# Kernel tuning notes

Hardware: AMD Instinct MI355X
Metric: run time of the kernel (lower is better)

Reference implementation:

```python
import jax, jax.numpy as jnp
import numpy as np

EMB_DIM = 2048
NUM_HEADS = 16
HEAD_DIM = EMB_DIM // NUM_HEADS  # 128
B, T = 4, 2048


def setup_inputs() -> dict:
    key = jax.random.key(0)
    ks = jax.random.split(key, 6)
    s = lambda fan_in: 1.0 / np.sqrt(fan_in)
    return {
        "x": jax.random.normal(ks[0], (B, T, EMB_DIM), dtype=jnp.float32),
        # weights stored [in, out] so forward is x @ W
        "Wq": jax.random.normal(ks[1], (EMB_DIM, EMB_DIM), dtype=jnp.float32) * s(EMB_DIM),
        "Wk": jax.random.normal(ks[2], (EMB_DIM, HEAD_DIM), dtype=jnp.float32) * s(EMB_DIM),
        "Wv": jax.random.normal(ks[3], (EMB_DIM, HEAD_DIM), dtype=jnp.float32) * s(EMB_DIM),
        "Wo": jax.random.normal(ks[4], (EMB_DIM, EMB_DIM), dtype=jnp.float32) * s(EMB_DIM),
        "bo": jax.random.normal(ks[5], (EMB_DIM,), dtype=jnp.float32) * 0.01,
    }


def reference(x, Wq, Wk, Wv, Wo, bo):
    Bsz, Tlen, C = x.shape
    H, D = NUM_HEADS, HEAD_DIM
    q = (x @ Wq).reshape(Bsz, Tlen, H, D)          # [B,T,H,D]
    k = x @ Wk                                      # [B,T,D] (single shared head)
    v = x @ Wv                                      # [B,T,D]
    # MQA: K/V broadcast over heads via einsum (no expand materialization)
    scores = jnp.einsum("bihd,bjd->bhij", q, k) / jnp.sqrt(jnp.float32(D))
    i = jnp.arange(Tlen)[:, None]
    j = jnp.arange(Tlen)[None, :]
    causal = j <= i                                  # attend to past & self
    scores = jnp.where(causal, scores, -jnp.inf)
    attn = jax.nn.softmax(scores, axis=-1)           # [B,H,T,T]
    out = jnp.einsum("bhij,bjd->bihd", attn, v).reshape(Bsz, Tlen, C)
    return out @ Wo + bo
```

## Files before the change

### kernel.cpp

```cpp
#include <hip/hip_runtime.h>
#include <stdint.h>

typedef __attribute__((ext_vector_type(8))) short short8;
typedef __attribute__((ext_vector_type(4))) float floatx4;

#define TLEN 2048
#define BATCH 4
#define EMB 2048
#define NHEADS 16
#define HDIM 128
#define MROWS (BATCH * TLEN)
#define QTILES (TLEN / 64)

__device__ __forceinline__ ushort f2bf(float f) {
    union { float f; uint32_t u; } v; v.f = f;
    uint32_t u = v.u;
    return (ushort)((u + 0x7fffu + ((u >> 16) & 1u)) >> 16);
}

__device__ __forceinline__ uint32_t cvt_pk_bf16(float a, float b) {
    uint32_t r;
    asm volatile("v_cvt_pk_bf16_f32 %0, %1, %2" : "=v"(r) : "v"(a), "v"(b));
    return r;
}

__device__ __forceinline__ void async_copy16(const ushort* g, ushort* l) {
    __builtin_amdgcn_global_load_lds(
        (const __attribute__((address_space(1))) uint32_t*)g,
        (__attribute__((address_space(3))) uint32_t*)l, 16, 0, 0);
}

__global__ __launch_bounds__(256) void cast_bf16_kernel(const float* __restrict__ in,
                                                        ushort* __restrict__ out, int n) {
    int i = (blockIdx.x * 256 + threadIdx.x) * 4;
    if (i >= n) return;
    float4 f = *(const float4*)(in + i);
    ushort4 o;
    o.x = f2bf(f.x); o.y = f2bf(f.y); o.z = f2bf(f.z); o.w = f2bf(f.w);
    *(ushort4*)(out + i) = o;
}

__global__ void transpose_cast_kernel(const float* __restrict__ in, ushort* __restrict__ out,
                                      int R, int Cc) {
    __shared__ float tile[32][33];
    int x = blockIdx.x * 32 + threadIdx.x;
    int y0 = blockIdx.y * 32;
#pragma unroll
    for (int i = 0; i < 4; i++) {
        int y = y0 + threadIdx.y + i * 8;
        tile[threadIdx.y + i * 8][threadIdx.x] = in[(size_t)y * Cc + x];
    }
    __syncthreads();
    int xo = y0 + threadIdx.x;
#pragma unroll
    for (int i = 0; i < 4; i++) {
        int yo = blockIdx.x * 32 + threadIdx.y + i * 8;
        out[(size_t)yo * R + xo] = f2bf(tile[threadIdx.x][threadIdx.y + i * 8]);
    }
}

template <int MODE>
__global__ __launch_bounds__(256) void gemm_bt_kernel(const ushort* __restrict__ A,
                                                      const ushort* __restrict__ Bt,
                                                      void* __restrict__ Cp,
                                                      void* __restrict__ Cp2,
                                                      const float* __restrict__ bias,
                                                      int M, int N, int K) {
    __shared__ ushort As[128 * 64];
    __shared__ ushort Bs[128 * 64];
    int tid = threadIdx.x;
    int wid = tid >> 6, lane = tid & 63;
    int quad = lane >> 4, l15 = lane & 15;

    int nwg = gridDim.x * gridDim.y;
    int wg = blockIdx.y * gridDim.x + blockIdx.x;
    int cpx = nwg >> 3;
    int swz = (wg & 7) * cpx + (wg >> 3);
    int bx = swz % gridDim.x, by = swz / gridDim.x;

    int m0 = by * 128;
    int n0 = bx * 128;
    int rm = (wid >> 1) * 64;
    int cn = (wid & 1) * 64;
    int grow = lane >> 3;
    int gcol = (lane & 7) * 8;

    floatx4 acc[4][4];
#pragma unroll
    for (int i = 0; i < 4; i++)
#pragma unroll
        for (int j = 0; j < 4; j++)
#pragma unroll
            for (int r = 0; r < 4; r++) acc[i][j][r] = 0.f;

    for (int kk = 0; kk < K; kk += 64) {
#pragma unroll
        for (int c = 0; c < 4; c++) {
            int chunk = wid * 4 + c;
            int row = chunk * 8 + grow;
            async_copy16(A + (size_t)(m0 + row) * K + kk + gcol, &As[chunk * 512]);
            async_copy16(Bt + (size_t)(n0 + row) * K + kk + gcol, &Bs[chunk * 512]);
        }
        __syncthreads();
#pragma unroll
        for (int ks = 0; ks < 64; ks += 32) {
            short8 af[4], bf[4];
#pragma unroll
            for (int i = 0; i < 4; i++)
                af[i] = *(const short8*)(&As[(rm + i * 16 + l15) * 64 + ks + quad * 8]);
#pragma unroll
            for (int j = 0; j < 4; j++)
                bf[j] = *(const short8*)(&Bs[(cn + j * 16 + l15) * 64 + ks + quad * 8]);
#pragma unroll
            for (int i = 0; i < 4; i++)
#pragma unroll
                for (int j = 0; j < 4; j++)
                    acc[i][j] = __builtin_amdgcn_mfma_f32_16x16x32_bf16(af[i], bf[j], acc[i][j], 0, 0, 0);
        }
        __syncthreads();
    }
#pragma unroll
    for (int i = 0; i < 4; i++)
#pragma unroll
        for (int j = 0; j < 4; j++) {
            if (MODE == 2 && n0 != 0) {
                int d = cn + j * 16 + l15;
                int row = m0 + rm + i * 16 + quad * 4;
                ushort4 o;
                o.x = f2bf(acc[i][j][0]); o.y = f2bf(acc[i][j][1]);
                o.z = f2bf(acc[i][j][2]); o.w = f2bf(acc[i][j][3]);
                *(ushort4*)((ushort*)Cp2 + (size_t)d * M + row) = o;
            } else {
#pragma unroll
                for (int r = 0; r < 4; r++) {
                    int row = m0 + rm + i * 16 + quad * 4 + r;
                    int col = n0 + cn + j * 16 + l15;
                    float v = acc[i][j][r];
                    if (MODE == 0) {
                        ((ushort*)Cp)[(size_t)row * N + col] = f2bf(v);
                    } else if (MODE == 1) {
                        ((float*)Cp)[(size_t)row * N + col] = v + bias[col];
                    } else {
                        ((ushort*)Cp)[(size_t)row * HDIM + col] = f2bf(v);
                    }
                }
            }
        }
}

__global__ __launch_bounds__(256, 2) void mqa_attn_kernel(const ushort* __restrict__ Qb,
                                                          const ushort* __restrict__ Kb,
                                                          const ushort* __restrict__ Vg,
                                                          ushort* __restrict__ Ab) {
    __shared__ ushort Ks[128 * 128];
    __shared__ ushort Vs[128 * 128];
    int tid = threadIdx.x;
    int wid = tid >> 6, lane = tid & 63;
    int quad = lane >> 4, l15 = lane & 15;
    int h0 = blockIdx.y * 2, b = blockIdx.z;
    int qt = (QTILES - 1) - blockIdx.x;
    const float scale2 = 0.08838834764831845f * 1.4426950408889634f;
    const ushort* kbase = Kb + (size_t)b * TLEN * HDIM;
    const ushort* vbase = Vg + (size_t)b * TLEN;
    size_t qrowbase = (size_t)b * TLEN + qt * 64;

    short8 aq[2][4];
#pragma unroll
    for (int hh = 0; hh < 2; hh++) {
        const ushort* qp = Qb + (qrowbase + wid * 16 + l15) * EMB + (h0 + hh) * HDIM + quad * 8;
#pragma unroll
        for (int kd = 0; kd < 4; kd++) aq[hh][kd] = *(const short8*)(qp + kd * 32);
    }

    float lsum[2] = {0.f, 0.f};
    floatx4 o_acc[2][8];
#pragma unroll
    for (int hh = 0; hh < 2; hh++)
#pragma unroll
        for (int nd = 0; nd < 8; nd++)
#pragma unroll
            for (int r = 0; r < 4; r++) o_acc[hh][nd][r] = 0.f;

    int rowloc = wid * 16 + l15;
    int dlim = rowloc + ((qt & 1) ? 64 : 0);
    int swz = (l15 & 7) << 3;
    int njt = qt / 2 + 1;
    bool evenqt = (qt & 1) == 0;

#pragma unroll 1
    for (int jt = 0; jt < njt; ++jt) {
#pragma unroll
        for (int i = 0; i < 8; i++) {
            int c = wid * 8 + i;
            int kr = c * 4 + (lane >> 4);
            int kc = ((lane & 15) * 8) ^ ((kr & 7) << 3);
            async_copy16(kbase + (size_t)(jt * 128 + kr) * HDIM + kc, &Ks[c * 512]);
            int vd = c * 4 + (lane >> 4);
            int vc = ((lane & 15) * 8) ^ ((vd & 7) << 3);
            async_copy16(vbase + (size_t)vd * MROWS + jt * 128 + vc, &Vs[c * 512]);
        }
        __syncthreads();

        bool diag = (jt == njt - 1);
#pragma unroll
        for (int jp = 0; jp < 4; jp++) {
            if (diag && evenqt && jp >= 2) continue;
            uint32_t XA[2][2], XB[2][2];
#pragma unroll
            for (int jj = 0; jj < 2; jj++) {
                int j = jp * 2 + jj;
                floatx4 s0, s1;
#pragma unroll
                for (int r = 0; r < 4; r++) { s0[r] = 0.f; s1[r] = 0.f; }
                __builtin_amdgcn_s_setprio(1);
#pragma unroll
                for (int kd = 0; kd < 4; kd++) {
                    short8 ak = *(const short8*)(&Ks[(j * 16 + l15) * 128 + ((kd * 32 + quad * 8) ^ swz)]);
                    s0 = __builtin_amdgcn_mfma_f32_16x16x32_bf16(ak, aq[0][kd], s0, 0, 0, 0);
                    s1 = __builtin_amdgcn_mfma_f32_16x16x32_bf16(ak, aq[1][kd], s1, 0, 0, 0);
                }
                __builtin_amdgcn_s_setprio(0);
                float e0[4], e1[4];
#pragma unroll
                for (int r = 0; r < 4; r++) {
                    int key = j * 16 + quad * 4 + r;
                    float v0 = exp2f(s0[r] * scale2);
                    float v1 = exp2f(s1[r] * scale2);
                    if (diag && key > dlim) { v0 = 0.f; v1 = 0.f; }
                    e0[r] = v0; e1[r] = v1;
                    lsum[0] += v0; lsum[1] += v1;
                }
                XA[0][jj] = cvt_pk_bf16(e0[0], e0[1]); XB[0][jj] = cvt_pk_bf16(e0[2], e0[3]);
                XA[1][jj] = cvt_pk_bf16(e1[0], e1[1]); XB[1][jj] = cvt_pk_bf16(e1[2], e1[3]);
            }
            short8 pf[2];
#pragma unroll
            for (int hh = 0; hh < 2; hh++) {
                uint32_t xA = XA[hh][0], yA = XA[hh][1];
                uint32_t xB = XB[hh][0], yB = XB[hh][1];
                asm volatile("v_permlane32_swap_b32 %0, %1" : "+v"(xA), "+v"(yA));
                asm volatile("v_permlane16_swap_b32 %0, %1" : "+v"(xA), "+v"(yA));
                asm volatile("v_permlane32_swap_b32 %0, %1" : "+v"(xB), "+v"(yB));
                asm volatile("v_permlane16_swap_b32 %0, %1" : "+v"(xB), "+v"(yB));
                union { uint32_t u[4]; short8 s; } fu;
                fu.u[0] = xA; fu.u[1] = xB; fu.u[2] = yA; fu.u[3] = yB;
                pf[hh] = fu.s;
            }
            __builtin_amdgcn_s_setprio(1);
#pragma unroll
            for (int nd = 0; nd < 8; nd++) {
                short8 vf = *(const short8*)(&Vs[(nd * 16 + l15) * 128 + ((jp * 32 + quad * 8) ^ swz)]);
                o_acc[0][nd] = __builtin_amdgcn_mfma_f32_16x16x32_bf16(pf[0], vf, o_acc[0][nd], 0, 0, 0);
                o_acc[1][nd] = __builtin_amdgcn_mfma_f32_16x16x32_bf16(pf[1], vf, o_acc[1][nd], 0, 0, 0);
            }
            __builtin_amdgcn_s_setprio(0);
        }
        __syncthreads();
    }

#pragma unroll
    for (int hh = 0; hh < 2; hh++) {
        float ls = lsum[hh];
        ls += __shfl_xor(ls, 16);
        ls += __shfl_xor(ls, 32);
        float inv_l[4];
#pragma unroll
        for (int r = 0; r < 4; r++) inv_l[r] = 1.f / __shfl(ls, quad * 4 + r, 16);
#pragma unroll
        for (int nd = 0; nd < 8; nd++)
#pragma unroll
            for (int r = 0; r < 4; r++) {
                size_t row = qrowbase + wid * 16 + quad * 4 + r;
                int col = (h0 + hh) * HDIM + nd * 16 + l15;
                Ab[row * EMB + col] = f2bf(o_acc[hh][nd][r] * inv_l[r]);
            }
    }
}

extern "C" void kernel_launch(void* const* d_in, const int* in_sizes, int n_in,
                              void* d_out, int out_size, void* d_ws, size_t ws_size,
                              hipStream_t stream) {
    const float* x  = (const float*)d_in[0];
    const float* Wq = (const float*)d_in[1];
    const float* Wk = (const float*)d_in[2];
    const float* Wv = (const float*)d_in[3];
    const float* Wo = (const float*)d_in[4];
    const float* bo = (const float*)d_in[5];
    float* out = (float*)d_out;

    ushort* ws = (ushort*)d_ws;
    ushort* Xb    = ws;
    ushort* Wq_t  = Xb    + (size_t)MROWS * EMB;
    ushort* Wkv_t = Wq_t  + (size_t)EMB * EMB;
    ushort* Wo_t  = Wkv_t + (size_t)256 * EMB;
    ushort* Qb    = Wo_t  + (size_t)EMB * EMB;
    ushort* Kb    = Qb    + (size_t)MROWS * EMB;
    ushort* Vg    = Kb    + (size_t)MROWS * HDIM;
    ushort* Ab    = Vg    + (size_t)HDIM * MROWS;

    cast_bf16_kernel<<<dim3(MROWS * EMB / 1024), 256, 0, stream>>>(x, Xb, MROWS * EMB);
    transpose_cast_kernel<<<dim3(EMB / 32, EMB / 32), dim3(32, 8), 0, stream>>>(Wq, Wq_t, EMB, EMB);
    transpose_cast_kernel<<<dim3(HDIM / 32, EMB / 32), dim3(32, 8), 0, stream>>>(Wk, Wkv_t, EMB, HDIM);
    transpose_cast_kernel<<<dim3(HDIM / 32, EMB / 32), dim3(32, 8), 0, stream>>>(Wv, Wkv_t + (size_t)HDIM * EMB, EMB, HDIM);
    transpose_cast_kernel<<<dim3(EMB / 32, EMB / 32), dim3(32, 8), 0, stream>>>(Wo, Wo_t, EMB, EMB);

    gemm_bt_kernel<0><<<dim3(EMB / 128, MROWS / 128), 256, 0, stream>>>(Xb, Wq_t, Qb, nullptr, nullptr, MROWS, EMB, EMB);
    gemm_bt_kernel<2><<<dim3(2, MROWS / 128), 256, 0, stream>>>(Xb, Wkv_t, Kb, Vg, nullptr, MROWS, 256, EMB);
    mqa_attn_kernel<<<dim3(QTILES, NHEADS / 2, BATCH), 256, 0, stream>>>(Qb, Kb, Vg, Ab);
    gemm_bt_kernel<1><<<dim3(EMB / 128, MROWS / 128), 256, 0, stream>>>(Ab, Wo_t, out, nullptr, bo, MROWS, EMB, EMB);
}
```

Before: 559.1 us.

## Pair causal q-tiles per attention block and split masked diagonal tile

Each attention workgroup now handles two query tiles, a late one and its mirrored early one, so every block does roughly equal causal work and the grid is halved. The diagonal key tile is compiled separately with masking, and all other tiles run without the per-element mask check. The GEMM kernel also drops its workgroup-index swizzle in favour of plain block indexing, which may change L2 reuse. With half as many blocks there may be fewer waves in flight, and the two tiles in a block run one after the other.

New measurement: 477.4 us. -14.6%, faster.

```diff
diff --git a/kernel.cpp b/kernel.cpp
--- a/kernel.cpp
+++ b/kernel.cpp
@@ -11,6 +11,9 @@
 #define HDIM 128
 #define MROWS (BATCH * TLEN)
 #define QTILES (TLEN / 64)
+
+struct TrueT  { static constexpr bool value = true;  };
+struct FalseT { static constexpr bool value = false; };
 
 __device__ __forceinline__ ushort f2bf(float f) {
     union { float f; uint32_t u; } v; v.f = f;
@@ -71,15 +74,8 @@
     int tid = threadIdx.x;
     int wid = tid >> 6, lane = tid & 63;
     int quad = lane >> 4, l15 = lane & 15;
-
-    int nwg = gridDim.x * gridDim.y;
-    int wg = blockIdx.y * gridDim.x + blockIdx.x;
-    int cpx = nwg >> 3;
-    int swz = (wg & 7) * cpx + (wg >> 3);
-    int bx = swz % gridDim.x, by = swz / gridDim.x;
-
-    int m0 = by * 128;
-    int n0 = bx * 128;
+    int m0 = blockIdx.y * 128;
+    int n0 = blockIdx.x * 128;
     int rm = (wid >> 1) * 64;
     int cn = (wid & 1) * 64;
     int grow = lane >> 3;
@@ -158,122 +154,141 @@
     int wid = tid >> 6, lane = tid & 63;
     int quad = lane >> 4, l15 = lane & 15;
     int h0 = blockIdx.y * 2, b = blockIdx.z;
-    int qt = (QTILES - 1) - blockIdx.x;
     const float scale2 = 0.08838834764831845f * 1.4426950408889634f;
     const ushort* kbase = Kb + (size_t)b * TLEN * HDIM;
     const ushort* vbase = Vg + (size_t)b * TLEN;
-    size_t qrowbase = (size_t)b * TLEN + qt * 64;
-
-    short8 aq[2][4];
-#pragma unroll
-    for (int hh = 0; hh < 2; hh++) {
-        const ushort* qp = Qb + (qrowbase + wid * 16 + l15) * EMB + (h0 + hh) * HDIM + quad * 8;
-#pragma unroll
-        for (int kd = 0; kd < 4; kd++) aq[hh][kd] = *(const short8*)(qp + kd * 32);
-    }
-
-    float lsum[2] = {0.f, 0.f};
-    floatx4 o_acc[2][8];
-#pragma unroll
-    for (int hh = 0; hh < 2; hh++)
-#pragma unroll
-        for (int nd = 0; nd < 8; nd++)
-#pragma unroll
-            for (int r = 0; r < 4; r++) o_acc[hh][nd][r] = 0.f;
 
     int rowloc = wid * 16 + l15;
-    int dlim = rowloc + ((qt & 1) ? 64 : 0);
     int swz = (l15 & 7) << 3;
-    int njt = qt / 2 + 1;
-    bool evenqt = (qt & 1) == 0;
-
-#pragma unroll 1
-    for (int jt = 0; jt < njt; ++jt) {
+
+    auto stage = [&](int jt) {
 #pragma unroll
         for (int i = 0; i < 8; i++) {
             int c = wid * 8 + i;
-            int kr = c * 4 + (lane >> 4);
-            int kc = ((lane & 15) * 8) ^ ((kr & 7) << 3);
+            int kr = c * 4 + quad;
+            int kc = (l15 * 8) ^ ((kr & 7) << 3);
             async_copy16(kbase + (size_t)(jt * 128 + kr) * HDIM + kc, &Ks[c * 512]);
-            int vd = c * 4 + (lane >> 4);
-            int vc = ((lane & 15) * 8) ^ ((vd & 7) << 3);
+            int vd = c * 4 + quad;
+            int vc = (l15 * 8) ^ ((vd & 7) << 3);
             async_copy16(vbase + (size_t)vd * MROWS + jt * 128 + vc, &Vs[c * 512]);
         }
-        __syncthreads();
-
-        bool diag = (jt == njt - 1);
-#pragma unroll
-        for (int jp = 0; jp < 4; jp++) {
-            if (diag && evenqt && jp >= 2) continue;
-            uint32_t XA[2][2], XB[2][2];
-#pragma unroll
-            for (int jj = 0; jj < 2; jj++) {
-                int j = jp * 2 + jj;
-                floatx4 s0, s1;
-#pragma unroll
-                for (int r = 0; r < 4; r++) { s0[r] = 0.f; s1[r] = 0.f; }
+    };
+
+#pragma unroll 1
+    for (int t = 0; t < 2; t++) {
+        int qt = (t == 0) ? (QTILES - 1 - blockIdx.x) : blockIdx.x;
+        size_t qrowbase = (size_t)b * TLEN + qt * 64;
+        int dlim = rowloc + ((qt & 1) ? 64 : 0);
+        bool evenqt = (qt & 1) == 0;
+        int njt = qt / 2 + 1;
+
+        short8 aq[2][4];
+#pragma unroll
+        for (int hh = 0; hh < 2; hh++) {
+            const ushort* qp = Qb + (qrowbase + wid * 16 + l15) * EMB + (h0 + hh) * HDIM + quad * 8;
+#pragma unroll
+            for (int kd = 0; kd < 4; kd++) aq[hh][kd] = *(const short8*)(qp + kd * 32);
+        }
+
+        float lsum[2] = {0.f, 0.f};
+        floatx4 o_acc[2][8];
+#pragma unroll
+        for (int hh = 0; hh < 2; hh++)
+#pragma unroll
+            for (int nd = 0; nd < 8; nd++)
+#pragma unroll
+                for (int r = 0; r < 4; r++) o_acc[hh][nd][r] = 0.f;
+
+        auto compute_tile = [&](auto mtag) {
+            constexpr bool MASKED = decltype(mtag)::value;
+#pragma unroll
+            for (int jp = 0; jp < 4; jp++) {
+                if (MASKED && evenqt && jp >= 2) continue;
+                uint32_t XA[2][2], XB[2][2];
+#pragma unroll
+                for (int jj = 0; jj < 2; jj++) {
+                    int j = jp * 2 + jj;
+                    floatx4 s0, s1;
+#pragma unroll
+                    for (int r = 0; r < 4; r++) { s0[r] = 0.f; s1[r] = 0.f; }
+                    __builtin_amdgcn_s_setprio(1);
+#pragma unroll
+                    for (int kd = 0; kd < 4; kd++) {
+                        short8 ak = *(const short8*)(&Ks[(j * 16 + l15) * 128 + ((kd * 32 + quad * 8) ^ swz)]);
+                        s0 = __builtin_amdgcn_mfma_f32_16x16x32_bf16(ak, aq[0][kd], s0, 0, 0, 0);
+                        s1 = __builtin_amdgcn_mfma_f32_16x16x32_bf16(ak, aq[1][kd], s1, 0, 0, 0);
+                    }
+                    __builtin_amdgcn_s_setprio(0);
+                    float e0[4], e1[4];
+#pragma unroll
+                    for (int r = 0; r < 4; r++) {
+                        float v0 = exp2f(s0[r] * scale2);
+                        float v1 = exp2f(s1[r] * scale2);
+                        if constexpr (MASKED) {
+                            int key = j * 16 + quad * 4 + r;
+                            if (key > dlim) { v0 = 0.f; v1 = 0.f; }
+                        }
+                        e0[r] = v0; e1[r] = v1;
+                        lsum[0] += v0; lsum[1] += v1;
+                    }
+                    XA[0][jj] = cvt_pk_bf16(e0[0], e0[1]); XB[0][jj] = cvt_pk_bf16(e0[2], e0[3]);
+                    XA[1][jj] = cvt_pk_bf16(e1[0], e1[1]); XB[1][jj] = cvt_pk_bf16(e1[2], e1[3]);
+                }
+                short8 pf[2];
+#pragma unroll
+                for (int hh = 0; hh < 2; hh++) {
+                    uint32_t xA = XA[hh][0], yA = XA[hh][1];
+                    uint32_t xB = XB[hh][0], yB = XB[hh][1];
+                    asm volatile("v_permlane32_swap_b32 %0, %1" : "+v"(xA), "+v"(yA));
+                    asm volatile("v_permlane16_swap_b32 %0, %1" : "+v"(xA), "+v"(yA));
+                    asm volatile("v_permlane32_swap_b32 %0, %1" : "+v"(xB), "+v"(yB));
+                    asm volatile("v_permlane16_swap_b32 %0, %1" : "+v"(xB), "+v"(yB));
+                    union { uint32_t u[4]; short8 s; } fu;
+                    fu.u[0] = xA; fu.u[1] = xB; fu.u[2] = yA; fu.u[3] = yB;
+                    pf[hh] = fu.s;
+                }
                 __builtin_amdgcn_s_setprio(1);
 #pragma unroll
-                for (int kd = 0; kd < 4; kd++) {
-                    short8 ak = *(const short8*)(&Ks[(j * 16 + l15) * 128 + ((kd * 32 + quad * 8) ^ swz)]);
-                    s0 = __builtin_amdgcn_mfma_f32_16x16x32_bf16(ak, aq[0][kd], s0, 0, 0, 0);
-                    s1 = __builtin_amdgcn_mfma_f32_16x16x32_bf16(ak, aq[1][kd], s1, 0, 0, 0);
+                for (int nd = 0; nd < 8; nd++) {
+                    short8 vf = *(const short8*)(&Vs[(nd * 16 + l15) * 128 + ((jp * 32 + quad * 8) ^ swz)]);
+                    o_acc[0][nd] = __builtin_amdgcn_mfma_f32_16x16x32_bf16(pf[0], vf, o_acc[0][nd], 0, 0, 0);
+                    o_acc[1][nd] = __builtin_amdgcn_mfma_f32_16x16x32_bf16(pf[1], vf, o_acc[1][nd], 0, 0, 0);
                 }
                 __builtin_amdgcn_s_setprio(0);
-                float e0[4], e1[4];
+            }
+        };
+
+#pragma unroll 1
+        for (int jt = 0; jt < njt - 1; ++jt) {
+            stage(jt);
+            __syncthreads();
+            compute_tile(FalseT{});
+            __syncthreads();
+        }
+        {
+            stage(njt - 1);
+            __syncthreads();
+            compute_tile(TrueT{});
+            __syncthreads();
+        }
+
+#pragma unroll
+        for (int hh = 0; hh < 2; hh++) {
+            float ls = lsum[hh];
+            ls += __shfl_xor(ls, 16);
+            ls += __shfl_xor(ls, 32);
+            float inv_l[4];
+#pragma unroll
+            for (int r = 0; r < 4; r++) inv_l[r] = 1.f / __shfl(ls, quad * 4 + r, 16);
+#pragma unroll
+            for (int nd = 0; nd < 8; nd++)
 #pragma unroll
                 for (int r = 0; r < 4; r++) {
-                    int key = j * 16 + quad * 4 + r;
-                    float v0 = exp2f(s0[r] * scale2);
-                    float v1 = exp2f(s1[r] * scale2);
-                    if (diag && key > dlim) { v0 = 0.f; v1 = 0.f; }
-                    e0[r] = v0; e1[r] = v1;
-                    lsum[0] += v0; lsum[1] += v1;
-                }
-                XA[0][jj] = cvt_pk_bf16(e0[0], e0[1]); XB[0][jj] = cvt_pk_bf16(e0[2], e0[3]);
-                XA[1][jj] = cvt_pk_bf16(e1[0], e1[1]); XB[1][jj] = cvt_pk_bf16(e1[2], e1[3]);
-            }
-            short8 pf[2];
-#pragma unroll
-            for (int hh = 0; hh < 2; hh++) {
-                uint32_t xA = XA[hh][0], yA = XA[hh][1];
-                uint32_t xB = XB[hh][0], yB = XB[hh][1];
-                asm volatile("v_permlane32_swap_b32 %0, %1" : "+v"(xA), "+v"(yA));
-                asm volatile("v_permlane16_swap_b32 %0, %1" : "+v"(xA), "+v"(yA));
-                asm volatile("v_permlane32_swap_b32 %0, %1" : "+v"(xB), "+v"(yB));
-                asm volatile("v_permlane16_swap_b32 %0, %1" : "+v"(xB), "+v"(yB));
-                union { uint32_t u[4]; short8 s; } fu;
-                fu.u[0] = xA; fu.u[1] = xB; fu.u[2] = yA; fu.u[3] = yB;
-                pf[hh] = fu.s;
-            }
-            __builtin_amdgcn_s_setprio(1);
-#pragma unroll
-            for (int nd = 0; nd < 8; nd++) {
-                short8 vf = *(const short8*)(&Vs[(nd * 16 + l15) * 128 + ((jp * 32 + quad * 8) ^ swz)]);
-                o_acc[0][nd] = __builtin_amdgcn_mfma_f32_16x16x32_bf16(pf[0], vf, o_acc[0][nd], 0, 0, 0);
-                o_acc[1][nd] = __builtin_amdgcn_mfma_f32_16x16x32_bf16(pf[1], vf, o_acc[1][nd], 0, 0, 0);
-            }
-            __builtin_amdgcn_s_setprio(0);
-        }
-        __syncthreads();
-    }
-
-#pragma unroll
-    for (int hh = 0; hh < 2; hh++) {
-        float ls = lsum[hh];
-        ls += __shfl_xor(ls, 16);
-        ls += __shfl_xor(ls, 32);
-        float inv_l[4];
-#pragma unroll
-        for (int r = 0; r < 4; r++) inv_l[r] = 1.f / __shfl(ls, quad * 4 + r, 16);
-#pragma unroll
-        for (int nd = 0; nd < 8; nd++)
-#pragma unroll
-            for (int r = 0; r < 4; r++) {
-                size_t row = qrowbase + wid * 16 + quad * 4 + r;
-                int col = (h0 + hh) * HDIM + nd * 16 + l15;
-                Ab[row * EMB + col] = f2bf(o_acc[hh][nd][r] * inv_l[r]);
-            }
+                    size_t row = qrowbase + wid * 16 + quad * 4 + r;
+                    int col = (h0 + hh) * HDIM + nd * 16 + l15;
+                    Ab[row * EMB + col] = f2bf(o_acc[hh][nd][r] * inv_l[r]);
+                }
+        }
     }
 }
 
@@ -306,6 +321,6 @@
 
     gemm_bt_kernel<0><<<dim3(EMB / 128, MROWS / 128), 256, 0, stream>>>(Xb, Wq_t, Qb, nullptr, nullptr, MROWS, EMB, EMB);
     gemm_bt_kernel<2><<<dim3(2, MROWS / 128), 256, 0, stream>>>(Xb, Wkv_t, Kb, Vg, nullptr, MROWS, 256, EMB);
-    mqa_attn_kernel<<<dim3(QTILES, NHEADS / 2, BATCH), 256, 0, stream>>>(Qb, Kb, Vg, Ab);
+    mqa_attn_kernel<<<dim3(QTILES / 2, NHEADS / 2, BATCH), 256, 0, stream>>>(Qb, Kb, Vg, Ab);
     gemm_bt_kernel<1><<<dim3(EMB / 128, MROWS / 128), 256, 0, stream>>>(Ab, Wo_t, out, nullptr, bo, MROWS, EMB, EMB);
 }
```
